# Performance work log

Hardware: AMD Instinct MI355X
Metric: run time of the kernel (lower is better)

The kernel has to match this reference:

```python
import jax, jax.numpy as jnp
import numpy as np

HIDDEN = 2048
N_HEADS = 16
N_KV_HEADS = 4
HEAD_DIM = HIDDEN // N_HEADS  # 128
N_GROUPS = N_HEADS // N_KV_HEADS  # 4
ROPE_THETA = 10000.0
B, S = 2, 2048


def setup_inputs() -> dict:
    key = jax.random.key(0)
    k1, k2, k3, k4, k5, k6 = jax.random.split(key, 6)
    hidden_states = jax.random.normal(k1, (B, S, HIDDEN), dtype=jnp.float32)
    position_ids = jnp.sort(jax.random.randint(k2, (B, S), 0, S), axis=-1).astype(jnp.int32)
    scale = 0.02
    Wq = jax.random.normal(k3, (HIDDEN, N_HEADS * HEAD_DIM), dtype=jnp.float32) * scale
    Wk = jax.random.normal(k4, (HIDDEN, N_KV_HEADS * HEAD_DIM), dtype=jnp.float32) * scale
    Wv = jax.random.normal(k5, (HIDDEN, N_KV_HEADS * HEAD_DIM), dtype=jnp.float32) * scale
    Wo = jax.random.normal(k6, (HIDDEN, HIDDEN), dtype=jnp.float32) * scale
    return {"hidden_states": hidden_states, "position_ids": position_ids,
            "Wq": Wq, "Wk": Wk, "Wv": Wv, "Wo": Wo}


def _rotate_half(x):
    x1, x2 = jnp.split(x, 2, axis=-1)
    return jnp.concatenate([-x2, x1], axis=-1)


def _rope_cos_sin(position_ids, dtype):
    # inv_freq: [HEAD_DIM/2]
    inv_freq = 1.0 / (ROPE_THETA ** (jnp.arange(0, HEAD_DIM, 2, dtype=jnp.float32) / HEAD_DIM))
    # freqs per position: [B, S, HEAD_DIM/2] -> duplicated to [B, S, HEAD_DIM]
    freqs = position_ids.astype(jnp.float32)[..., None] * inv_freq  # [B,S,Dh/2]
    emb = jnp.concatenate([freqs, freqs], axis=-1)  # [B,S,Dh]
    cos = jnp.cos(emb)[:, None, :, :].astype(dtype)  # [B,1,S,Dh]
    sin = jnp.sin(emb)[:, None, :, :].astype(dtype)
    return cos, sin


def reference(hidden_states, position_ids, Wq, Wk, Wv, Wo):
    b, s, _ = hidden_states.shape
    dtype = hidden_states.dtype
    q = (hidden_states @ Wq).reshape(b, s, N_HEADS, HEAD_DIM).transpose(0, 2, 1, 3)      # [B,Hq,S,Dh]
    k = (hidden_states @ Wk).reshape(b, s, N_KV_HEADS, HEAD_DIM).transpose(0, 2, 1, 3)   # [B,Hkv,S,Dh]
    v = (hidden_states @ Wv).reshape(b, s, N_KV_HEADS, HEAD_DIM).transpose(0, 2, 1, 3)

    cos, sin = _rope_cos_sin(position_ids, dtype)
    q = q * cos + _rotate_half(q) * sin
    k = k * cos + _rotate_half(k) * sin

    # repeat_kv: [B,Hkv,S,Dh] -> [B,Hq,S,Dh] (repeat-interleave along head axis)
    k = jnp.repeat(k, N_GROUPS, axis=1)
    v = jnp.repeat(v, N_GROUPS, axis=1)

    scores = jnp.einsum('bhqd,bhkd->bhqk', q, k) / jnp.sqrt(jnp.asarray(HEAD_DIM, dtype))
    # causal additive mask
    causal = jnp.tril(jnp.ones((s, s), dtype=bool))
    scores = jnp.where(causal[None, None], scores, jnp.asarray(-1e9, dtype))
    probs = jax.nn.softmax(scores, axis=-1)
    attn = jnp.einsum('bhqk,bhkd->bhqd', probs, v)  # [B,Hq,S,Dh]
    attn = attn.transpose(0, 2, 1, 3).reshape(b, s, HIDDEN)
    return attn @ Wo
```

## Files before the change

kernel.cpp:

```cpp
#include <hip/hip_runtime.h>
#include <math.h>

#define HID 2048
#define NH 16
#define NKV 4
#define DH 128
#define BB 2
#define SS 2048
#define ROWS (BB*SS)
#define NQKV 3072
#define KOFF 2048
#define VOFF 2560

typedef float f32x4 __attribute__((ext_vector_type(4)));
typedef float f32x16 __attribute__((ext_vector_type(16)));
typedef __bf16 bf16x8 __attribute__((ext_vector_type(8)));
typedef unsigned short ushortx8 __attribute__((ext_vector_type(8)));
typedef unsigned short ushortx4 __attribute__((ext_vector_type(4)));
typedef float floatx4 __attribute__((ext_vector_type(4)));

__device__ __forceinline__ float b2f(unsigned short u) {
  union { float f; unsigned int i; } x; x.i = ((unsigned int)u) << 16; return x.f;
}
__device__ __forceinline__ unsigned short f2b(float f) {
  union { float f; unsigned int i; } x; x.f = f;
  unsigned int r = x.i + 0x7fffu + ((x.i >> 16) & 1u);
  return (unsigned short)(r >> 16);
}

__device__ __forceinline__ void gload16(const void* g, void* l) {
  __builtin_amdgcn_global_load_lds(
      (__attribute__((address_space(1))) void*)(void*)(g),
      (__attribute__((address_space(3))) void*)(l), 16, 0, 0);
}

__device__ __forceinline__ void wgbar() {
  asm volatile("" ::: "memory");
  __builtin_amdgcn_s_barrier();
  asm volatile("" ::: "memory");
}
#define VMCNT4 asm volatile("s_waitcnt vmcnt(4)" ::: "memory")
#define VMCNT0 asm volatile("s_waitcnt vmcnt(0)" ::: "memory")

__device__ __forceinline__ unsigned cvtpk(float lo, float hi_) {
  unsigned r;
  asm("v_cvt_pk_bf16_f32 %0, %1, %2" : "=v"(r) : "v"(lo), "v"(hi_));
  return r;
}
__device__ __forceinline__ void plswap(unsigned& x, unsigned& y) {
  asm volatile("v_permlane32_swap_b32 %0, %1" : "+v"(x), "+v"(y));
}

__global__ __launch_bounds__(256) void cast_f32_bf16(const float* __restrict__ in,
                                                     unsigned short* __restrict__ out, int n4) {
  int i = blockIdx.x * 256 + threadIdx.x;
  if (i >= n4) return;
  floatx4 v = ((const floatx4*)in)[i];
  ushortx4 o;
  o.x = f2b(v.x); o.y = f2b(v.y); o.z = f2b(v.z); o.w = f2b(v.w);
  ((ushortx4*)out)[i] = o;
}

__global__ __launch_bounds__(256) void tcast(const float* __restrict__ W,
                                             unsigned short* __restrict__ Wt, int K, int N) {
  __shared__ float t[64][65];
  int tid = threadIdx.x;
  int k0 = blockIdx.y * 64, n0 = blockIdx.x * 64;
#pragma unroll
  for (int u0 = 0; u0 < 1024; u0 += 256) {
    int u = u0 + tid;
    int r = u >> 4, c4 = (u & 15) * 4;
    floatx4 v = *(const floatx4*)(const void*)&W[(size_t)(k0 + r) * N + n0 + c4];
    t[r][c4 + 0] = v.x; t[r][c4 + 1] = v.y; t[r][c4 + 2] = v.z; t[r][c4 + 3] = v.w;
  }
  __syncthreads();
#pragma unroll
  for (int u0 = 0; u0 < 512; u0 += 256) {
    int u = u0 + tid;
    int n = u >> 3, g = (u & 7) * 8;
    ushortx8 o;
#pragma unroll
    for (int k2 = 0; k2 < 8; ++k2) o[k2] = f2b(t[g + k2][n]);
    *(ushortx8*)(void*)&Wt[(size_t)(n0 + n) * K + k0 + g] = o;
  }
}

template <int BF16OUT>
__global__ __launch_bounds__(512, 1) void gemm256(const unsigned short* __restrict__ A,
                                                  const unsigned short* __restrict__ Bt,
                                                  void* __restrict__ Cv, int M, int N, int K) {
  __shared__ __align__(16) unsigned char smem[131072];
  const int tid = threadIdx.x;
  const int wave = tid >> 6, lane = tid & 63;
  const int fr = lane & 15, fq = lane >> 4;
  const int wm = wave >> 2, wn = wave & 3;

  const int ntn = N >> 8;
  const int cpx = gridDim.x >> 3;
  const int wg = (blockIdx.x & 7) * cpx + (blockIdx.x >> 3);
  const int m0 = (wg / ntn) << 8, n0 = (wg % ntn) << 8;
  const int NT = K >> 6;

  const int l8 = lane >> 3, l7 = lane & 7;
  const size_t srcOff = (size_t)(wave * 8 + l8) * K + ((l7 ^ l8) * 8);
  const unsigned short* Ag = A + (size_t)m0 * K;
  const unsigned short* Bg = Bt + (size_t)n0 * K;

  const int colx0 = (fq * 16) ^ ((fr & 7) << 4);
  const int colx1 = (64 + fq * 16) ^ ((fr & 7) << 4);
  const int aRow = (wm * 128 + fr) * 128;
  const int bRow = (wn * 64 + fr) * 128;

#define STAGE_A(kt2, mh)                                                                   \
  { const unsigned short* gp = Ag + (size_t)((mh) * 128) * K + (size_t)(kt2) * 64 + srcOff; \
    char* lp = (char*)smem + (((kt2) & 1) * 65536) + (mh) * 16384 + wave * 1024;            \
    gload16(gp, lp);                                                                        \
    gload16(gp + (size_t)64 * K, lp + 8192); }

#define STAGE_B(kt2, nh)                                                                   \
  { const unsigned short* gp = Bg + (size_t)((nh) * 128) * K + (size_t)(kt2) * 64 + srcOff; \
    char* lp = (char*)smem + (((kt2) & 1) * 65536) + 32768 + (nh) * 16384 + wave * 1024;    \
    gload16(gp, lp);                                                                        \
    gload16(gp + (size_t)64 * K, lp + 8192); }

  f32x4 acc[8][4] = {};
  bf16x8 aF[4][2], b0F[2][2], b1F[2][2];

#define LDA(mh)                                                                 \
  { const char* base_ = (const char*)smem + cur * 65536 + aRow;                 \
    _Pragma("unroll") for (int mi = 0; mi < 4; ++mi) {                          \
      aF[mi][0] = *(const bf16x8*)(const void*)(base_ + ((mh)*4 + mi) * 2048 + colx0); \
      aF[mi][1] = *(const bf16x8*)(const void*)(base_ + ((mh)*4 + mi) * 2048 + colx1); } }

#define LDB(nh, BF)                                                             \
  { const char* base_ = (const char*)smem + cur * 65536 + 32768 + bRow;         \
    _Pragma("unroll") for (int ni = 0; ni < 2; ++ni) {                          \
      BF[ni][0] = *(const bf16x8*)(const void*)(base_ + ((nh)*2 + ni) * 2048 + colx0); \
      BF[ni][1] = *(const bf16x8*)(const void*)(base_ + ((nh)*2 + ni) * 2048 + colx1); } }

#define MM(mh, nh, BF)                                                          \
  { __builtin_amdgcn_s_setprio(1);                                              \
    _Pragma("unroll") for (int mi = 0; mi < 4; ++mi)                            \
    _Pragma("unroll") for (int ni = 0; ni < 2; ++ni) {                          \
      acc[(mh)*4+mi][(nh)*2+ni] = __builtin_amdgcn_mfma_f32_16x16x32_bf16(      \
          aF[mi][0], BF[ni][0], acc[(mh)*4+mi][(nh)*2+ni], 0, 0, 0);            \
      acc[(mh)*4+mi][(nh)*2+ni] = __builtin_amdgcn_mfma_f32_16x16x32_bf16(      \
          aF[mi][1], BF[ni][1], acc[(mh)*4+mi][(nh)*2+ni], 0, 0, 0); }          \
    __builtin_amdgcn_s_setprio(0); }

  STAGE_A(0, 0); STAGE_A(0, 1); STAGE_B(0, 0); STAGE_B(0, 1);
  STAGE_B(1, 0); STAGE_B(1, 1);
  VMCNT4;
  wgbar();

  for (int kt = 0; kt < NT; ++kt) {
    const int cur = kt & 1;
    LDA(0); LDB(0, b0F);
    if (kt + 1 < NT) STAGE_A(kt + 1, 0);
    wgbar();
    MM(0, 0, b0F);
    wgbar();
    LDB(1, b1F);
    if (kt + 1 < NT) STAGE_A(kt + 1, 1);
    wgbar();
    MM(0, 1, b1F);
    wgbar();
    LDA(1);
    if (kt + 2 < NT) STAGE_B(kt + 2, 0);
    wgbar();
    MM(1, 0, b0F);
    wgbar();
    if (kt + 2 < NT) { STAGE_B(kt + 2, 1); VMCNT4; }
    else if (kt + 1 < NT) { VMCNT0; }
    wgbar();
    MM(1, 1, b1F);
    wgbar();
  }

#pragma unroll
  for (int mi = 0; mi < 8; ++mi)
#pragma unroll
    for (int ni = 0; ni < 4; ++ni)
#pragma unroll
      for (int r = 0; r < 4; ++r) {
        size_t row = (size_t)(m0 + wm * 128 + mi * 16 + fq * 4 + r);
        size_t col = (size_t)(n0 + wn * 64 + ni * 16 + fr);
        if (BF16OUT)
          ((unsigned short*)Cv)[row * N + col] = f2b(acc[mi][ni][r]);
        else
          ((float*)Cv)[row * N + col] = acc[mi][ni][r];
      }
#undef STAGE_A
#undef STAGE_B
#undef LDA
#undef LDB
#undef MM
}

template <int BF16OUT>
__global__ __launch_bounds__(512, 1) void gemm128n(const unsigned short* __restrict__ A,
                                                   const unsigned short* __restrict__ Bt,
                                                   void* __restrict__ Cv, int M, int N, int K) {
  __shared__ __align__(16) unsigned char smem[98304];
  const int tid = threadIdx.x;
  const int wave = tid >> 6, lane = tid & 63;
  const int fr = lane & 15, fq = lane >> 4;
  const int wm = wave & 3, wn = wave >> 2;

  const int ntn = N >> 8;
  const int cpx = gridDim.x >> 3;
  const int wg = (blockIdx.x & 7) * cpx + (blockIdx.x >> 3);
  const int m0 = (wg / ntn) << 7, n0 = (wg % ntn) << 8;
  const int NT = K >> 6;

  const int l8 = lane >> 3, l7 = lane & 7;
  const size_t srcOff = (size_t)(wave * 8 + l8) * K + ((l7 ^ l8) * 8);
  const unsigned short* Ag = A + (size_t)m0 * K;
  const unsigned short* Bg = Bt + (size_t)n0 * K;

  const int cx0 = (fq * 16) ^ ((fr & 7) << 4);
  const int cx1 = (64 + fq * 16) ^ ((fr & 7) << 4);
  const int aRow = (wm * 32 + fr) * 128;
  const int bRow = (wn * 128 + fr) * 128;

#define SA(kt2)  { const unsigned short* gp = Ag + (size_t)(kt2) * 64 + srcOff;             \
    char* lp = (char*)smem + (((kt2) & 1) * 49152) + wave * 1024;                           \
    gload16(gp, lp);  gload16(gp + (size_t)64 * K, lp + 8192); }
#define SB01(kt2) { const unsigned short* gp = Bg + (size_t)(kt2) * 64 + srcOff;            \
    char* lp = (char*)smem + (((kt2) & 1) * 49152) + 16384 + wave * 1024;                   \
    gload16(gp, lp);  gload16(gp + (size_t)64 * K, lp + 8192); }
#define SB23(kt2) { const unsigned short* gp = Bg + (size_t)128 * K + (size_t)(kt2) * 64 + srcOff; \
    char* lp = (char*)smem + (((kt2) & 1) * 49152) + 32768 + wave * 1024;                   \
    gload16(gp, lp);  gload16(gp + (size_t)64 * K, lp + 8192); }

  f32x4 acc[2][8] = {};
  bf16x8 aFk[2], bF0[4][2], bF1[4][2];

#define LDAK(kf) { const char* b_ = (const char*)smem + cur * 49152 + aRow;                 \
    aFk[0] = *(const bf16x8*)(const void*)(b_ + ((kf) ? cx1 : cx0));                        \
    aFk[1] = *(const bf16x8*)(const void*)(b_ + 2048 + ((kf) ? cx1 : cx0)); }
#define LDB4(BF, nb) { const char* b_ = (const char*)smem + cur * 49152 + 16384 + bRow + (nb) * 8192; \
    _Pragma("unroll") for (int ni = 0; ni < 4; ++ni) {                                      \
      BF[ni][0] = *(const bf16x8*)(const void*)(b_ + ni * 2048 + cx0);                      \
      BF[ni][1] = *(const bf16x8*)(const void*)(b_ + ni * 2048 + cx1); } }
#define MM8(BF, no, kf) { __builtin_amdgcn_s_setprio(1);                                    \
    _Pragma("unroll") for (int mi = 0; mi < 2; ++mi)                                        \
    _Pragma("unroll") for (int ni = 0; ni < 4; ++ni)                                        \
      acc[mi][(no) + ni] = __builtin_amdgcn_mfma_f32_16x16x32_bf16(                         \
          aFk[mi], BF[ni][kf], acc[mi][(no) + ni], 0, 0, 0);                                \
    __builtin_amdgcn_s_setprio(0); }

  SA(0); SB01(0); SB23(0); SB01(1); SB23(1);
  VMCNT4;
  wgbar();

  for (int kt = 0; kt < NT; ++kt) {
    const int cur = kt & 1;
    LDAK(0); LDB4(bF0, 0); LDB4(bF1, 1);
    if (kt + 1 < NT) SA(kt + 1);
    wgbar();
    MM8(bF0, 0, 0); MM8(bF1, 4, 0);
    wgbar();
    LDAK(1);
    if (kt + 2 < NT) { SB01(kt + 2); SB23(kt + 2); VMCNT4; }
    else if (kt + 1 < NT) { VMCNT0; }
    wgbar();
    MM8(bF0, 0, 1); MM8(bF1, 4, 1);
    wgbar();
  }

#pragma unroll
  for (int mi = 0; mi < 2; ++mi)
#pragma unroll
    for (int ni = 0; ni < 8; ++ni)
#pragma unroll
      for (int r = 0; r < 4; ++r) {
        size_t row = (size_t)(m0 + wm * 32 + mi * 16 + fq * 4 + r);
        size_t col = (size_t)(n0 + wn * 128 + ni * 16 + fr);
        if (BF16OUT)
          ((unsigned short*)Cv)[row * N + col] = f2b(acc[mi][ni][r]);
        else
          ((float*)Cv)[row * N + col] = acc[mi][ni][r];
      }
#undef SA
#undef SB01
#undef SB23
#undef LDAK
#undef LDB4
#undef MM8
}

__global__ __launch_bounds__(256) void rope_kernel(unsigned short* __restrict__ QKV,
                                                   const int* __restrict__ pos) {
  int bs = blockIdx.x;
  int t = threadIdx.x;
  __shared__ float cs[64], sn[64];
  if (t < 64) {
    float p = (float)pos[bs];
    float inv = expf(-(float)t * 0.14391156831212787f);
    sincosf(p * inv, &sn[t], &cs[t]);
  }
  __syncthreads();
  unsigned short* row = QKV + (size_t)bs * NQKV;
  for (int u = t; u < 320; u += 256) {
    int h = u >> 4, d0 = (u & 15) * 4;
    int col = (h < 16) ? h * DH : KOFF + (h - 16) * DH;
    float sc = (h < 16) ? 0.08838834764831845f : 1.0f;
    ushortx4 lo = *(const ushortx4*)(const void*)(row + col + d0);
    ushortx4 hi = *(const ushortx4*)(const void*)(row + col + 64 + d0);
    ushortx4 olo, ohi;
#pragma unroll
    for (int k = 0; k < 4; ++k) {
      float x1 = b2f(lo[k]), x2 = b2f(hi[k]);
      float c = cs[d0 + k], s = sn[d0 + k];
      olo[k] = f2b((x1 * c - x2 * s) * sc);
      ohi[k] = f2b((x2 * c + x1 * s) * sc);
    }
    *(ushortx4*)(void*)(row + col + d0) = olo;
    *(ushortx4*)(void*)(row + col + 64 + d0) = ohi;
  }
}

__global__ __launch_bounds__(256) void vtrans(const unsigned short* __restrict__ QKV,
                                              unsigned short* __restrict__ Vt) {
  __shared__ unsigned short t[32][34];
  int s0 = blockIdx.x * 32, d0 = blockIdx.y * 32;
  int bh = blockIdx.z; int b = bh >> 2, h = bh & 3;
  int tx = threadIdx.x & 31, ty = threadIdx.x >> 5;
  const unsigned short* src = QKV + (size_t)b * SS * NQKV + VOFF + h * DH;
  for (int i = 0; i < 32; i += 8)
    t[ty + i][tx] = src[(size_t)(s0 + ty + i) * NQKV + d0 + tx];
  __syncthreads();
  unsigned short* dst = Vt + ((size_t)(b * NKV + h) * DH) * SS;
  for (int i = 0; i < 32; i += 8)
    dst[(size_t)(d0 + ty + i) * SS + s0 + tx] = t[tx][ty + i];
}

__global__ __launch_bounds__(256, 2) void attn_kernel(const unsigned short* __restrict__ QKV,
                                                      const unsigned short* __restrict__ Vt,
                                                      unsigned short* __restrict__ Out) {
  int id = blockIdx.x;
  int g = id & 7;
  int b = g >> 2, hkv = g & 3;
  int r3 = id >> 3;
  int hsub = (r3 >> 2) & 3;
  int h = hkv * 4 + hsub;
  int q0 = (r3 & 3) | (((r3 >> 4) & 1) << 2);
  int qt = (r3 >> 5) ? (15 - q0) : q0;
  int tid = threadIdx.x;
  int w = tid >> 6, lane = tid & 63;
  int l31 = lane & 31, hi = lane >> 5;

  __shared__ __align__(16) unsigned short K_lds[2][64 * 128];
  __shared__ __align__(16) unsigned short V_lds[2][128 * 64];
  __shared__ float lsum_lds[4][32];

  const unsigned short* Kbase = QKV + (size_t)b * SS * NQKV + KOFF + hkv * DH;
  const unsigned short* Vbase = Vt + (size_t)(b * NKV + hkv) * DH * SS;

  int kr4 = lane >> 4, kc = lane & 15;
  int vr8 = lane >> 3, vc = lane & 7;

#define STAGE(kv0, buf)                                                                  \
  { _Pragma("unroll") for (int i = 0; i < 4; ++i) {                                      \
      int r0 = w * 16 + i * 4; int row = r0 + kr4;                                       \
      gload16(Kbase + (size_t)((kv0) + row) * NQKV + ((kc ^ (row & 7)) * 8),             \
              (char*)K_lds[buf] + r0 * 256); }                                           \
    _Pragma("unroll") for (int i = 0; i < 4; ++i) {                                      \
      int r0 = w * 32 + i * 8; int row = r0 + vr8;                                       \
      gload16(Vbase + (size_t)row * SS + (kv0) + ((vc ^ (row & 7)) * 8),                 \
              (char*)V_lds[buf] + r0 * 128); } }

  const unsigned short* Qp =
      QKV + (size_t)((size_t)b * SS + qt * 128 + w * 32 + l31) * NQKV + h * DH + hi * 8;
  bf16x8 qf[8];
#pragma unroll
  for (int ks = 0; ks < 8; ++ks) qf[ks] = *(const bf16x8*)(const void*)(Qp + ks * 16);

  f32x16 o[4] = {};
  float lsum = 0.f;
  int lsw = (l31 & 7) << 4;
  int nt = 2 * qt + 2;

  STAGE(0, 0);
  VMCNT0;
  wgbar();
  int cur = 0;

  for (int t = 0; t < nt; ++t) {
    if (t + 1 < nt) STAGE((t + 1) * 64, cur ^ 1);

    f32x16 s0 = {}, s1 = {};
    {
      const char* kb = (const char*)K_lds[cur];
      __builtin_amdgcn_s_setprio(1);
#pragma unroll
      for (int ks = 0; ks < 8; ++ks) {
        int co = (ks * 32 + hi * 16) ^ lsw;
        bf16x8 k0 = *(const bf16x8*)(const void*)(kb + l31 * 256 + co);
        bf16x8 k1 = *(const bf16x8*)(const void*)(kb + (32 + l31) * 256 + co);
        s0 = __builtin_amdgcn_mfma_f32_32x32x16_bf16(k0, qf[ks], s0, 0, 0, 0);
        s1 = __builtin_amdgcn_mfma_f32_32x32x16_bf16(k1, qf[ks], s1, 0, 0, 0);
      }
      __builtin_amdgcn_s_setprio(0);
    }

    float p0[16], p1[16];
    float ps = 0.f;
    if (t >= 2 * qt) {
      int qrel = w * 32 + l31 - (t - 2 * qt) * 64;
#pragma unroll
      for (int r = 0; r < 16; ++r) {
        int kvr = (r & 3) + 8 * (r >> 2) + 4 * hi;
        float e0 = __expf(s0[r]), e1 = __expf(s1[r]);
        p0[r] = (kvr <= qrel) ? e0 : 0.f;
        p1[r] = (kvr + 32 <= qrel) ? e1 : 0.f;
        ps += p0[r] + p1[r];
      }
    } else {
#pragma unroll
      for (int r = 0; r < 16; ++r) {
        p0[r] = __expf(s0[r]); p1[r] = __expf(s1[r]);
        ps += p0[r] + p1[r];
      }
    }
    lsum += ps;

    union U8 { unsigned u[4]; bf16x8 v; } fa[4];
    {
      unsigned a0 = cvtpk(p0[0], p0[1]),  a1 = cvtpk(p0[2], p0[3]);
      unsigned a2 = cvtpk(p0[4], p0[5]),  a3 = cvtpk(p0[6], p0[7]);
      plswap(a0, a2); plswap(a1, a3);
      fa[0].u[0] = a0; fa[0].u[1] = a1; fa[0].u[2] = a2; fa[0].u[3] = a3;
      unsigned a4 = cvtpk(p0[8], p0[9]),   a5 = cvtpk(p0[10], p0[11]);
      unsigned a6 = cvtpk(p0[12], p0[13]), a7 = cvtpk(p0[14], p0[15]);
      plswap(a4, a6); plswap(a5, a7);
      fa[1].u[0] = a4; fa[1].u[1] = a5; fa[1].u[2] = a6; fa[1].u[3] = a7;
      unsigned b0 = cvtpk(p1[0], p1[1]),  b1 = cvtpk(p1[2], p1[3]);
      unsigned b2 = cvtpk(p1[4], p1[5]),  b3 = cvtpk(p1[6], p1[7]);
      plswap(b0, b2); plswap(b1, b3);
      fa[2].u[0] = b0; fa[2].u[1] = b1; fa[2].u[2] = b2; fa[2].u[3] = b3;
      unsigned b4 = cvtpk(p1[8], p1[9]),   b5 = cvtpk(p1[10], p1[11]);
      unsigned b6 = cvtpk(p1[12], p1[13]), b7 = cvtpk(p1[14], p1[15]);
      plswap(b4, b6); plswap(b5, b7);
      fa[3].u[0] = b4; fa[3].u[1] = b5; fa[3].u[2] = b6; fa[3].u[3] = b7;
    }

    __builtin_amdgcn_s_setprio(1);
#pragma unroll
    for (int dblk = 0; dblk < 4; ++dblk) {
      const char* vrow = (const char*)V_lds[cur] + (dblk * 32 + l31) * 128;
#pragma unroll
      for (int ks = 0; ks < 4; ++ks) {
        bf16x8 vb = *(const bf16x8*)(const void*)(vrow + ((ks * 32 + hi * 16) ^ lsw));
        o[dblk] = __builtin_amdgcn_mfma_f32_32x32x16_bf16(fa[ks].v, vb, o[dblk], 0, 0, 0);
      }
    }
    __builtin_amdgcn_s_setprio(0);

    VMCNT0;
    wgbar();
    cur ^= 1;
  }
#undef STAGE

  float ls = lsum + __shfl_xor(lsum, 32);
  if (hi == 0) lsum_lds[w][l31] = ls;
  __syncthreads();
  size_t obase = (size_t)((size_t)b * SS + qt * 128 + w * 32) * HID + h * DH + l31;
#pragma unroll
  for (int r = 0; r < 16; ++r) {
    int qr = (r & 3) + 8 * (r >> 2) + 4 * hi;
    float inv = 1.0f / lsum_lds[w][qr];
    size_t orow = obase + (size_t)qr * HID;
#pragma unroll
    for (int dblk = 0; dblk < 4; ++dblk)
      Out[orow + dblk * 32] = f2b(o[dblk][r] * inv);
  }
}

extern "C" void kernel_launch(void* const* d_in, const int* in_sizes, int n_in,
                              void* d_out, int out_size, void* d_ws, size_t ws_size,
                              hipStream_t stream) {
  const float* hs = (const float*)d_in[0];
  const int* pos = (const int*)d_in[1];
  const float* Wq = (const float*)d_in[2];
  const float* Wk = (const float*)d_in[3];
  const float* Wv = (const float*)d_in[4];
  const float* Wo = (const float*)d_in[5];

  char* ws = (char*)d_ws;
  size_t off = 0;
  unsigned short* hsb = (unsigned short*)(ws + off); off += (size_t)ROWS * HID * 2;
  unsigned short* WqkvT = (unsigned short*)(ws + off); off += (size_t)NQKV * HID * 2;
  unsigned short* WoT = (unsigned short*)(ws + off); off += (size_t)HID * HID * 2;
  unsigned short* QKV = (unsigned short*)(ws + off); off += (size_t)ROWS * NQKV * 2;
  unsigned short* Vtb = (unsigned short*)(ws + off); off += (size_t)BB * NKV * DH * SS * 2;

  cast_f32_bf16<<<(ROWS * HID / 4 + 255) / 256, 256, 0, stream>>>(hs, hsb, ROWS * HID / 4);
  tcast<<<dim3(HID / 64, HID / 64), 256, 0, stream>>>(Wq, WqkvT, HID, HID);
  tcast<<<dim3(512 / 64, HID / 64), 256, 0, stream>>>(Wk, WqkvT + (size_t)2048 * 2048, HID, 512);
  tcast<<<dim3(512 / 64, HID / 64), 256, 0, stream>>>(Wv, WqkvT + (size_t)2560 * 2048, HID, 512);
  tcast<<<dim3(HID / 64, HID / 64), 256, 0, stream>>>(Wo, WoT, HID, HID);

  gemm256<1><<<(ROWS / 256) * (NQKV / 256), 512, 0, stream>>>(hsb, WqkvT, QKV, ROWS, NQKV, HID);
  rope_kernel<<<ROWS, 256, 0, stream>>>(QKV, pos);
  vtrans<<<dim3(SS / 32, DH / 32, BB * NKV), 256, 0, stream>>>(QKV, Vtb);
  attn_kernel<<<512, 256, 0, stream>>>(QKV, Vtb, hsb);
  gemm128n<0><<<(ROWS / 128) * (HID / 256), 512, 0, stream>>>(hsb, WoT, d_out, ROWS, HID, HID);
}
```

Before: 197.2 us.

## Retile QKV GEMM to 256x192 tiles and fuse QKV weight transpose-casts

Replaces the 256x256 QKV GEMM with a 256x192 tile (4x2 wave layout, 64x96 per wave). This gives 256 workgroups instead of 192, so every CU gets one tile, and the k-loop is restructured into two half-k phases with all B fragments loaded up front. The three Q/K/V weight transpose-cast launches are merged into one kernel, and the rope kernel uses 8-wide vectors with fewer threads. The smaller N tile lowers per-workgroup arithmetic intensity and uses more registers for B fragments.

```diff
diff --git a/kernel.cpp b/kernel.cpp
--- a/kernel.cpp
+++ b/kernel.cpp
@@ -40,6 +40,7 @@
   asm volatile("" ::: "memory");
 }
 #define VMCNT4 asm volatile("s_waitcnt vmcnt(4)" ::: "memory")
+#define VMCNT3 asm volatile("s_waitcnt vmcnt(3)" ::: "memory")
 #define VMCNT0 asm volatile("s_waitcnt vmcnt(0)" ::: "memory")
 
 __device__ __forceinline__ unsigned cvtpk(float lo, float hi_) {
@@ -61,6 +62,38 @@
   ((ushortx4*)out)[i] = o;
 }
 
+__global__ __launch_bounds__(256) void tcast3(const float* __restrict__ Wq,
+                                              const float* __restrict__ Wk,
+                                              const float* __restrict__ Wv,
+                                              unsigned short* __restrict__ Wt) {
+  __shared__ float t[64][65];
+  int tid = threadIdx.x;
+  int bx = blockIdx.x;
+  const float* W; int N, n0; unsigned short* dst;
+  if (bx < 32)      { W = Wq; N = 2048; n0 = bx * 64;        dst = Wt; }
+  else if (bx < 40) { W = Wk; N = 512;  n0 = (bx - 32) * 64; dst = Wt + (size_t)2048 * 2048; }
+  else              { W = Wv; N = 512;  n0 = (bx - 40) * 64; dst = Wt + (size_t)2560 * 2048; }
+  int k0 = blockIdx.y * 64;
+  const int K = HID;
+#pragma unroll
+  for (int u0 = 0; u0 < 1024; u0 += 256) {
+    int u = u0 + tid;
+    int r = u >> 4, c4 = (u & 15) * 4;
+    floatx4 v = *(const floatx4*)(const void*)&W[(size_t)(k0 + r) * N + n0 + c4];
+    t[r][c4 + 0] = v.x; t[r][c4 + 1] = v.y; t[r][c4 + 2] = v.z; t[r][c4 + 3] = v.w;
+  }
+  __syncthreads();
+#pragma unroll
+  for (int u0 = 0; u0 < 512; u0 += 256) {
+    int u = u0 + tid;
+    int n = u >> 3, g = (u & 7) * 8;
+    ushortx8 o;
+#pragma unroll
+    for (int k2 = 0; k2 < 8; ++k2) o[k2] = f2b(t[g + k2][n]);
+    *(ushortx8*)(void*)&dst[(size_t)(n0 + n) * K + k0 + g] = o;
+  }
+}
+
 __global__ __launch_bounds__(256) void tcast(const float* __restrict__ W,
                                              unsigned short* __restrict__ Wt, int K, int N) {
   __shared__ float t[64][65];
@@ -86,19 +119,19 @@
 }
 
 template <int BF16OUT>
-__global__ __launch_bounds__(512, 1) void gemm256(const unsigned short* __restrict__ A,
-                                                  const unsigned short* __restrict__ Bt,
-                                                  void* __restrict__ Cv, int M, int N, int K) {
+__global__ __launch_bounds__(512, 1) void gemm192n(const unsigned short* __restrict__ A,
+                                                   const unsigned short* __restrict__ Bt,
+                                                   void* __restrict__ Cv, int M, int N, int K) {
   __shared__ __align__(16) unsigned char smem[131072];
   const int tid = threadIdx.x;
   const int wave = tid >> 6, lane = tid & 63;
   const int fr = lane & 15, fq = lane >> 4;
-  const int wm = wave >> 2, wn = wave & 3;
-
-  const int ntn = N >> 8;
+  const int wm = wave & 3, wn = wave >> 2;
+
+  const int ntn = N / 192;
   const int cpx = gridDim.x >> 3;
   const int wg = (blockIdx.x & 7) * cpx + (blockIdx.x >> 3);
-  const int m0 = (wg / ntn) << 8, n0 = (wg % ntn) << 8;
+  const int m0 = (wg / ntn) << 8, n0 = (wg % ntn) * 192;
   const int NT = K >> 6;
 
   const int l8 = lane >> 3, l7 = lane & 7;
@@ -106,95 +139,74 @@
   const unsigned short* Ag = A + (size_t)m0 * K;
   const unsigned short* Bg = Bt + (size_t)n0 * K;
 
-  const int colx0 = (fq * 16) ^ ((fr & 7) << 4);
-  const int colx1 = (64 + fq * 16) ^ ((fr & 7) << 4);
-  const int aRow = (wm * 128 + fr) * 128;
-  const int bRow = (wn * 64 + fr) * 128;
-
-#define STAGE_A(kt2, mh)                                                                   \
-  { const unsigned short* gp = Ag + (size_t)((mh) * 128) * K + (size_t)(kt2) * 64 + srcOff; \
-    char* lp = (char*)smem + (((kt2) & 1) * 65536) + (mh) * 16384 + wave * 1024;            \
-    gload16(gp, lp);                                                                        \
-    gload16(gp + (size_t)64 * K, lp + 8192); }
-
-#define STAGE_B(kt2, nh)                                                                   \
-  { const unsigned short* gp = Bg + (size_t)((nh) * 128) * K + (size_t)(kt2) * 64 + srcOff; \
-    char* lp = (char*)smem + (((kt2) & 1) * 65536) + 32768 + (nh) * 16384 + wave * 1024;    \
-    gload16(gp, lp);                                                                        \
-    gload16(gp + (size_t)64 * K, lp + 8192); }
-
-  f32x4 acc[8][4] = {};
-  bf16x8 aF[4][2], b0F[2][2], b1F[2][2];
-
-#define LDA(mh)                                                                 \
-  { const char* base_ = (const char*)smem + cur * 65536 + aRow;                 \
-    _Pragma("unroll") for (int mi = 0; mi < 4; ++mi) {                          \
-      aF[mi][0] = *(const bf16x8*)(const void*)(base_ + ((mh)*4 + mi) * 2048 + colx0); \
-      aF[mi][1] = *(const bf16x8*)(const void*)(base_ + ((mh)*4 + mi) * 2048 + colx1); } }
-
-#define LDB(nh, BF)                                                             \
-  { const char* base_ = (const char*)smem + cur * 65536 + 32768 + bRow;         \
-    _Pragma("unroll") for (int ni = 0; ni < 2; ++ni) {                          \
-      BF[ni][0] = *(const bf16x8*)(const void*)(base_ + ((nh)*2 + ni) * 2048 + colx0); \
-      BF[ni][1] = *(const bf16x8*)(const void*)(base_ + ((nh)*2 + ni) * 2048 + colx1); } }
-
-#define MM(mh, nh, BF)                                                          \
-  { __builtin_amdgcn_s_setprio(1);                                              \
-    _Pragma("unroll") for (int mi = 0; mi < 4; ++mi)                            \
-    _Pragma("unroll") for (int ni = 0; ni < 2; ++ni) {                          \
-      acc[(mh)*4+mi][(nh)*2+ni] = __builtin_amdgcn_mfma_f32_16x16x32_bf16(      \
-          aF[mi][0], BF[ni][0], acc[(mh)*4+mi][(nh)*2+ni], 0, 0, 0);            \
-      acc[(mh)*4+mi][(nh)*2+ni] = __builtin_amdgcn_mfma_f32_16x16x32_bf16(      \
-          aF[mi][1], BF[ni][1], acc[(mh)*4+mi][(nh)*2+ni], 0, 0, 0); }          \
+  const int cx0 = (fq * 16) ^ ((fr & 7) << 4);
+  const int cx1 = (64 + fq * 16) ^ ((fr & 7) << 4);
+  const int aRow = (wm * 64 + fr) * 128;
+  const int bRow = (wn * 96 + fr) * 128;
+
+#define SA(kt2)  { const unsigned short* gp = Ag + (size_t)(kt2) * 64 + srcOff;              \
+    char* lp = (char*)smem + (((kt2) & 1) * 65536) + wave * 1024;                            \
+    gload16(gp, lp);                 gload16(gp + (size_t)64 * K, lp + 8192);                \
+    gload16(gp + (size_t)128 * K, lp + 16384); gload16(gp + (size_t)192 * K, lp + 24576); }
+#define SB(kt2)  { const unsigned short* gp = Bg + (size_t)(kt2) * 64 + srcOff;              \
+    char* lp = (char*)smem + (((kt2) & 1) * 65536) + 32768 + wave * 1024;                    \
+    gload16(gp, lp);  gload16(gp + (size_t)64 * K, lp + 8192);                               \
+    gload16(gp + (size_t)128 * K, lp + 16384); }
+
+  f32x4 acc[4][6] = {};
+  bf16x8 aF0[4], aF1[4], bF[6][2];
+
+#define LDA(kf, AF) { const char* b_ = (const char*)smem + cur * 65536 + aRow;               \
+    _Pragma("unroll") for (int mi = 0; mi < 4; ++mi)                                         \
+      AF[mi] = *(const bf16x8*)(const void*)(b_ + mi * 2048 + ((kf) ? cx1 : cx0)); }
+#define LDBALL { const char* b_ = (const char*)smem + cur * 65536 + 32768 + bRow;            \
+    _Pragma("unroll") for (int ni = 0; ni < 6; ++ni) {                                       \
+      bF[ni][0] = *(const bf16x8*)(const void*)(b_ + ni * 2048 + cx0);                       \
+      bF[ni][1] = *(const bf16x8*)(const void*)(b_ + ni * 2048 + cx1); } }
+#define MM24(AF, kf) { __builtin_amdgcn_s_setprio(1);                                        \
+    _Pragma("unroll") for (int mi = 0; mi < 4; ++mi)                                         \
+    _Pragma("unroll") for (int ni = 0; ni < 6; ++ni)                                         \
+      acc[mi][ni] = __builtin_amdgcn_mfma_f32_16x16x32_bf16(                                 \
+          AF[mi], bF[ni][kf], acc[mi][ni], 0, 0, 0);                                         \
     __builtin_amdgcn_s_setprio(0); }
 
-  STAGE_A(0, 0); STAGE_A(0, 1); STAGE_B(0, 0); STAGE_B(0, 1);
-  STAGE_B(1, 0); STAGE_B(1, 1);
-  VMCNT4;
+  SA(0); SB(0); SB(1);
+  VMCNT3;
   wgbar();
 
   for (int kt = 0; kt < NT; ++kt) {
     const int cur = kt & 1;
-    LDA(0); LDB(0, b0F);
-    if (kt + 1 < NT) STAGE_A(kt + 1, 0);
-    wgbar();
-    MM(0, 0, b0F);
-    wgbar();
-    LDB(1, b1F);
-    if (kt + 1 < NT) STAGE_A(kt + 1, 1);
-    wgbar();
-    MM(0, 1, b1F);
-    wgbar();
-    LDA(1);
-    if (kt + 2 < NT) STAGE_B(kt + 2, 0);
-    wgbar();
-    MM(1, 0, b0F);
-    wgbar();
-    if (kt + 2 < NT) { STAGE_B(kt + 2, 1); VMCNT4; }
+    LDA(0, aF0); LDBALL;
+    if (kt + 1 < NT) SA(kt + 1);
+    wgbar();
+    MM24(aF0, 0);
+    wgbar();
+    LDA(1, aF1);
+    if (kt + 2 < NT) { SB(kt + 2); VMCNT3; }
     else if (kt + 1 < NT) { VMCNT0; }
     wgbar();
-    MM(1, 1, b1F);
-    wgbar();
-  }
-
-#pragma unroll
-  for (int mi = 0; mi < 8; ++mi)
-#pragma unroll
-    for (int ni = 0; ni < 4; ++ni)
+    MM24(aF1, 1);
+    wgbar();
+  }
+
+#pragma unroll
+  for (int mi = 0; mi < 4; ++mi)
+#pragma unroll
+    for (int ni = 0; ni < 6; ++ni)
 #pragma unroll
       for (int r = 0; r < 4; ++r) {
-        size_t row = (size_t)(m0 + wm * 128 + mi * 16 + fq * 4 + r);
-        size_t col = (size_t)(n0 + wn * 64 + ni * 16 + fr);
+        size_t row = (size_t)(m0 + wm * 64 + mi * 16 + fq * 4 + r);
+        size_t col = (size_t)(n0 + wn * 96 + ni * 16 + fr);
         if (BF16OUT)
           ((unsigned short*)Cv)[row * N + col] = f2b(acc[mi][ni][r]);
         else
           ((float*)Cv)[row * N + col] = acc[mi][ni][r];
       }
-#undef STAGE_A
-#undef STAGE_B
+#undef SA
+#undef SB
 #undef LDA
-#undef LDB
-#undef MM
+#undef LDBALL
+#undef MM24
 }
 
 template <int BF16OUT>
@@ -302,22 +314,22 @@
   }
   __syncthreads();
   unsigned short* row = QKV + (size_t)bs * NQKV;
-  for (int u = t; u < 320; u += 256) {
-    int h = u >> 4, d0 = (u & 15) * 4;
+  if (t < 160) {
+    int h = t >> 3, d0 = (t & 7) * 8;
     int col = (h < 16) ? h * DH : KOFF + (h - 16) * DH;
     float sc = (h < 16) ? 0.08838834764831845f : 1.0f;
-    ushortx4 lo = *(const ushortx4*)(const void*)(row + col + d0);
-    ushortx4 hi = *(const ushortx4*)(const void*)(row + col + 64 + d0);
-    ushortx4 olo, ohi;
-#pragma unroll
-    for (int k = 0; k < 4; ++k) {
+    ushortx8 lo = *(const ushortx8*)(const void*)(row + col + d0);
+    ushortx8 hi = *(const ushortx8*)(const void*)(row + col + 64 + d0);
+    ushortx8 olo, ohi;
+#pragma unroll
+    for (int k = 0; k < 8; ++k) {
       float x1 = b2f(lo[k]), x2 = b2f(hi[k]);
       float c = cs[d0 + k], s = sn[d0 + k];
       olo[k] = f2b((x1 * c - x2 * s) * sc);
       ohi[k] = f2b((x2 * c + x1 * s) * sc);
     }
-    *(ushortx4*)(void*)(row + col + d0) = olo;
-    *(ushortx4*)(void*)(row + col + 64 + d0) = ohi;
+    *(ushortx8*)(void*)(row + col + d0) = olo;
+    *(ushortx8*)(void*)(row + col + 64 + d0) = ohi;
   }
 }
 
@@ -498,12 +510,10 @@
   unsigned short* Vtb = (unsigned short*)(ws + off); off += (size_t)BB * NKV * DH * SS * 2;
 
   cast_f32_bf16<<<(ROWS * HID / 4 + 255) / 256, 256, 0, stream>>>(hs, hsb, ROWS * HID / 4);
-  tcast<<<dim3(HID / 64, HID / 64), 256, 0, stream>>>(Wq, WqkvT, HID, HID);
-  tcast<<<dim3(512 / 64, HID / 64), 256, 0, stream>>>(Wk, WqkvT + (size_t)2048 * 2048, HID, 512);
-  tcast<<<dim3(512 / 64, HID / 64), 256, 0, stream>>>(Wv, WqkvT + (size_t)2560 * 2048, HID, 512);
+  tcast3<<<dim3(48, HID / 64), 256, 0, stream>>>(Wq, Wk, Wv, WqkvT);
   tcast<<<dim3(HID / 64, HID / 64), 256, 0, stream>>>(Wo, WoT, HID, HID);
 
-  gemm256<1><<<(ROWS / 256) * (NQKV / 256), 512, 0, stream>>>(hsb, WqkvT, QKV, ROWS, NQKV, HID);
+  gemm192n<1><<<(ROWS / 256) * (NQKV / 192), 512, 0, stream>>>(hsb, WqkvT, QKV, ROWS, NQKV, HID);
   rope_kernel<<<ROWS, 256, 0, stream>>>(QKV, pos);
   vtrans<<<dim3(SS / 32, DH / 32, BB * NKV), 256, 0, stream>>>(QKV, Vtb);
   attn_kernel<<<512, 256, 0, stream>>>(QKV, Vtb, hsb);
```

After: 185.1 us. 1.07x faster.
